# Kernel tuning notes

Hardware: AMD Instinct MI355X
Metric: run time of the kernel (lower is better)

The kernel has to match this reference:

```python
import jax, jax.numpy as jnp
import numpy as np

EPS = 1e-6


def setup_inputs() -> dict:
    key = jax.random.key(0)
    ks = jax.random.split(key, 7)
    T, B, D, N = 512, 32, 1024, 128
    scale_w = (6.0 / (N + D)) ** 0.5  # xavier_uniform bound
    def w(k):
        return jax.random.uniform(k, (N, D), jnp.float32, -scale_w, scale_w)
    return {
        "x": jax.random.normal(ks[0], (T, B, D), jnp.float32),
        "S0": jnp.zeros((B, N, N), jnp.float32),
        "W_k": w(ks[1]),
        "W_v": w(ks[2]),
        "W_q": w(ks[3]),
        "W_erase": w(ks[4]),
        "W_write": w(ks[5]),
    }


def _ntm_forward(x, S0, W_k, W_v, W_q, W_erase, W_write):
    # Projections for all timesteps at once: (T, B, n_state)
    k = jnp.einsum('tbd,nd->tbn', x, W_k)
    v = jnp.einsum('tbd,nd->tbn', x, W_v)
    q = jnp.einsum('tbd,nd->tbn', x, W_q)
    erase = jnp.einsum('tbd,nd->tbn', x, W_erase)  # use_sigmoid=False: raw
    write = jnp.einsum('tbd,nd->tbn', x, W_write)

    def step(S, inp):
        k_t, v_t, q_t, e_t, w_t = inp
        k_norm = k_t / (jnp.linalg.norm(k_t, axis=-1, keepdims=True) + EPS)
        # S: (B, n, n); outer products via broadcasting
        erase_outer = e_t[:, :, None] * k_norm[:, None, :]
        write_outer = (w_t * v_t)[:, :, None] * k_norm[:, None, :]
        S_new = jnp.tanh(S * (1.0 - erase_outer) + write_outer)
        Sq = jnp.einsum('bij,bj->bi', S_new, q_t)
        out = Sq * jax.nn.silu(Sq)
        return S_new, out

    S_final, outputs = jax.lax.scan(step, S0, (k, v, q, erase, write))
    return outputs, S_final


def reference(x, S0, W_k, W_v, W_q, W_erase, W_write):
    return _ntm_forward(x, S0, W_k, W_v, W_q, W_erase, W_write)
```

## Files before the change

kernel.cpp:

```cpp
#include <hip/hip_runtime.h>
#include <hip/hip_bf16.h>


typedef __attribute__((ext_vector_type(8))) short bf16x8;
typedef __attribute__((ext_vector_type(4))) float f32x4;
typedef __attribute__((ext_vector_type(2))) float f32x2;
typedef __attribute__((ext_vector_type(4))) unsigned short u16x4;

static constexpr int T_STEPS = 512;
static constexpr int BATCH   = 32;
static constexpr int DDIM    = 1024;
static constexpr int NDIM    = 128;
static constexpr int LDC     = 5 * NDIM;
static constexpr int MROWS   = T_STEPS * BATCH;
static constexpr int OUT_N   = T_STEPS * BATCH * NDIM;

__device__ __forceinline__ unsigned short rne_bf16(float v) {
    unsigned u = __builtin_bit_cast(unsigned, v);
    u += 0x7FFFu + ((u >> 16) & 1u);
    return (unsigned short)(u >> 16);
}

static constexpr int LSTR = 40;
static constexpr int OA = 0, OB = 128 * LSTR;

__global__ __launch_bounds__(256, 3) void gemm3_kernel(
    const float* __restrict__ x,
    const float* __restrict__ w0, const float* __restrict__ w1,
    const float* __restrict__ w2, const float* __restrict__ w3,
    const float* __restrict__ w4,
    float* __restrict__ C)
{
    __shared__ unsigned short lds[2 * 128 * LSTR];

    const float* Ws[5] = {w0, w1, w2, w3, w4};
    const int id  = blockIdx.x;
    const int xcd = id & 7;
    const int kq  = id >> 3;
    const int bn  = kq % 5;
    const int bm  = (kq / 5) * 8 + xcd;

    const int tid  = threadIdx.x;
    const int wave = tid >> 6, lane = tid & 63;
    const int quad = lane >> 4, l16 = lane & 15;
    const int wm = (wave >> 1) * 64, wn = (wave & 1) * 64;
    const int m0 = bm * 128;
    const float* wsrc = Ws[bn];

    f32x4 acc[4][4];
#pragma unroll
    for (int i = 0; i < 4; ++i)
#pragma unroll
        for (int j = 0; j < 4; ++j) acc[i][j] = (f32x4)(0.0f);

    const int srow = tid >> 3;
    const int sc4  = tid & 7;
    const int fa = (wm + l16) * LSTR + quad * 8;
    const int fb = (wn + l16) * LSTR + quad * 8;

    const float* xp[4];
    const float* wp[4];
#pragma unroll
    for (int i = 0; i < 4; ++i) {
        xp[i] = x    + (size_t)(m0 + srow + i * 32) * DDIM + sc4 * 4;
        wp[i] = wsrc + (size_t)(srow + i * 32) * DDIM + sc4 * 4;
    }

    f32x4 ra[4], rb[4];
#pragma unroll
    for (int i = 0; i < 4; ++i) { ra[i] = *(const f32x4*)xp[i]; rb[i] = *(const f32x4*)wp[i]; }

    for (int kk = 0; kk < 32; ++kk) {
#pragma unroll
        for (int i = 0; i < 4; ++i) {
            u16x4 ha, hb;
#pragma unroll
            for (int j = 0; j < 4; ++j) {
                ha[j] = rne_bf16(ra[i][j]);
                hb[j] = rne_bf16(rb[i][j]);
            }
            const int o = (srow + i * 32) * LSTR + sc4 * 4;
            *(u16x4*)&lds[OA + o] = ha;
            *(u16x4*)&lds[OB + o] = hb;
        }
        __syncthreads();

        const int kn = (kk + 1 < 32) ? kk + 1 : 31;
#pragma unroll
        for (int i = 0; i < 4; ++i) {
            ra[i] = *(const f32x4*)(xp[i] + kn * 32);
            rb[i] = *(const f32x4*)(wp[i] + kn * 32);
        }

        bf16x8 ah[4], bh[4];
#pragma unroll
        for (int i = 0; i < 4; ++i) {
            ah[i] = *(const bf16x8*)&lds[OA + fa + i * 16 * LSTR];
            bh[i] = *(const bf16x8*)&lds[OB + fb + i * 16 * LSTR];
        }
#pragma unroll
        for (int mi = 0; mi < 4; ++mi)
#pragma unroll
            for (int ni = 0; ni < 4; ++ni)
                acc[mi][ni] = __builtin_amdgcn_mfma_f32_16x16x32_bf16(
                    ah[mi], bh[ni], acc[mi][ni], 0, 0, 0);
        __syncthreads();
    }

#pragma unroll
    for (int mi = 0; mi < 4; ++mi)
#pragma unroll
        for (int ni = 0; ni < 4; ++ni) {
            const int row = m0 + wm + mi * 16 + quad * 4;
            const int col = bn * 128 + wn + ni * 16 + l16;
#pragma unroll
            for (int r = 0; r < 4; ++r)
                C[(size_t)(row + r) * LDC + col] = acc[mi][ni][r];
        }
}

__global__ __launch_bounds__(256) void knorm_kernel(float* __restrict__ C)
{
    const int r    = blockIdx.x * 4 + (threadIdx.x >> 6);
    const int lane = threadIdx.x & 63;
    float* base = C + (size_t)r * LDC;

    f32x2 k2 = *(const f32x2*)(base + lane * 2);
    f32x2 v2 = *(const f32x2*)(base + NDIM + lane * 2);
    f32x2 w2 = *(const f32x2*)(base + 4 * NDIM + lane * 2);

    float ss = k2.x * k2.x + k2.y * k2.y;
#pragma unroll
    for (int off = 32; off >= 1; off >>= 1) ss += __shfl_xor(ss, off, 64);
    float inv = __builtin_amdgcn_rcpf(sqrtf(ss) + 1e-6f);

    f32x2 kn = {k2.x * inv, k2.y * inv};
    f32x2 wv = {v2.x * w2.x, v2.y * w2.y};
    *(f32x2*)(base + lane * 2) = kn;
    *(f32x2*)(base + NDIM + lane * 2) = wv;
}

__device__ __forceinline__ float tanh_fast(float xx) {
    float ex = __builtin_amdgcn_exp2f(xx * 2.8853900817779268f);
    float r  = __builtin_amdgcn_rcpf(ex + 1.0f);
    return fmaf(-2.0f, r, 1.0f);
}

template <int CTRL, int RMASK>
__device__ __forceinline__ float dpp_add(float x) {
    int yi = __builtin_amdgcn_update_dpp(
        0, __builtin_bit_cast(int, x), CTRL, RMASK, 0xF, true);
    return x + __builtin_bit_cast(float, yi);
}

__device__ __forceinline__ float dpp_reduce32(float x) {
    x = dpp_add<0xB1,  0xF>(x);
    x = dpp_add<0x4E,  0xF>(x);
    x = dpp_add<0x141, 0xF>(x);
    x = dpp_add<0x140, 0xF>(x);
    x = dpp_add<0x142, 0xA>(x);
    return x;
}

__global__ __launch_bounds__(256) void ntm_scan_kernel(
    const float* __restrict__ C, const float* __restrict__ S0,
    float* __restrict__ out)
{
    const int L    = blockIdx.x;
    const int b    = (L & 7) + 8 * ((L >> 3) & 3);
    const int row  = (L >> 5) * 8 + (threadIdx.x >> 5);
    const int g    = threadIdx.x & 31;
    const int col0 = g * 4;

    f32x4 S = *(const f32x4*)(S0 + ((size_t)b * NDIM + row) * NDIM + col0);

    const size_t STRIDE = (size_t)BATCH * LDC;
    const float* pb = C + (size_t)b * LDC;

    f32x4 kS[8], qS[8];
    float eS[8], wvS[8];

#pragma unroll
    for (int s = 0; s < 4; ++s) {
        const float* p = pb + (size_t)s * STRIDE;
        kS[s]  = *(const f32x4*)(p + col0);
        qS[s]  = *(const f32x4*)(p + 2 * NDIM + col0);
        eS[s]  = p[3 * NDIM + row];
        wvS[s] = p[NDIM + row];
    }

    float* op = out + (size_t)b * NDIM + row;

    for (int ti = 0; ti < T_STEPS / 8; ++ti) {
#pragma unroll
        for (int j = 0; j < 8; ++j) {
            const int t = ti * 8 + j;
            {
                int tp = t + 4;
                if (tp > T_STEPS - 1) tp = T_STEPS - 1;
                const float* p = pb + (size_t)tp * STRIDE;
                const int ps = (j + 4) & 7;
                kS[ps]  = *(const f32x4*)(p + col0);
                qS[ps]  = *(const f32x4*)(p + 2 * NDIM + col0);
                eS[ps]  = p[3 * NDIM + row];
                wvS[ps] = p[NDIM + row];
            }
            float dot = 0.0f;
#pragma unroll
            for (int u = 0; u < 4; ++u) {
                float t0  = fmaf(-eS[j], S[u], wvS[j]);
                float pre = fmaf(kS[j][u], t0, S[u]);
                S[u] = tanh_fast(pre);
                dot = fmaf(S[u], qS[j][u], dot);
            }
            dot = dpp_reduce32(dot);

            if ((threadIdx.x & 31) == 31)
                op[(size_t)t * BATCH * NDIM] = dot;
        }
    }

    *(f32x4*)(out + (size_t)T_STEPS * BATCH * NDIM
              + ((size_t)b * NDIM + row) * NDIM + col0) = S;
}

__global__ __launch_bounds__(256) void silu_kernel(float* __restrict__ out)
{
    const int i = blockIdx.x * 256 + threadIdx.x;
    f32x4 d = ((const f32x4*)out)[i];
    f32x4 y;
#pragma unroll
    for (int j = 0; j < 4; ++j) {
        float sg = __builtin_amdgcn_rcpf(
            1.0f + __builtin_amdgcn_exp2f(-d[j] * 1.4426950408889634f));
        y[j] = d[j] * d[j] * sg;
    }
    ((f32x4*)out)[i] = y;
}

extern "C" void kernel_launch(void* const* d_in, const int* in_sizes, int n_in,
                              void* d_out, int out_size, void* d_ws, size_t ws_size,
                              hipStream_t stream) {
    const float* x  = (const float*)d_in[0];
    const float* S0 = (const float*)d_in[1];
    const float* wk = (const float*)d_in[2];
    const float* wv = (const float*)d_in[3];
    const float* wq = (const float*)d_in[4];
    const float* we = (const float*)d_in[5];
    const float* ww = (const float*)d_in[6];
    float* out = (float*)d_out;
    float* C   = (float*)d_ws;

    gemm3_kernel<<<640, 256, 0, stream>>>(x, wk, wv, wq, we, ww, C);
    knorm_kernel<<<MROWS / 4, 256, 0, stream>>>(C);
    ntm_scan_kernel<<<512, 256, 0, stream>>>(C, S0, out);
    silu_kernel<<<OUT_N / 1024, 256, 0, stream>>>(out);
}
```

Before: 276.3 us.

## Pre-convert weights to bf16 fragment layout, restructure GEMM, fuse SiLU into scan

Adds a kernel that converts the five weight matrices to bf16 once, stored in an MFMA-fragment-ordered layout. The GEMM is replaced by one where each 512-thread block holds a 64-row slab of x in swizzled LDS and computes all five projections, reading B fragments straight from global memory with double buffering. The SiLU gating is fused into the scan's output write, which removes a separate pass over the output, and the scan's prefetch depth drops from 4 to 2 steps. Risks include low occupancy from 128KB of LDS per block, only 256 blocks, and uncached B fragment loads from global memory.

```diff
diff --git a/kernel.cpp b/kernel.cpp
--- a/kernel.cpp
+++ b/kernel.cpp
@@ -6,6 +6,7 @@
 typedef __attribute__((ext_vector_type(4))) float f32x4;
 typedef __attribute__((ext_vector_type(2))) float f32x2;
 typedef __attribute__((ext_vector_type(4))) unsigned short u16x4;
+typedef __attribute__((ext_vector_type(8))) unsigned short u16x8;
 
 static constexpr int T_STEPS = 512;
 static constexpr int BATCH   = 32;
@@ -15,107 +16,133 @@
 static constexpr int MROWS   = T_STEPS * BATCH;
 static constexpr int OUT_N   = T_STEPS * BATCH * NDIM;
 
+static constexpr size_t C_BYTES = (size_t)MROWS * LDC * 4;
+
 __device__ __forceinline__ unsigned short rne_bf16(float v) {
     unsigned u = __builtin_bit_cast(unsigned, v);
     u += 0x7FFFu + ((u >> 16) & 1u);
     return (unsigned short)(u >> 16);
 }
 
-static constexpr int LSTR = 40;
-static constexpr int OA = 0, OB = 128 * LSTR;
-
-__global__ __launch_bounds__(256, 3) void gemm3_kernel(
-    const float* __restrict__ x,
+__global__ __launch_bounds__(256) void wconv_kernel(
     const float* __restrict__ w0, const float* __restrict__ w1,
     const float* __restrict__ w2, const float* __restrict__ w3,
     const float* __restrict__ w4,
+    unsigned short* __restrict__ W2)
+{
+    const int idx = blockIdx.x * 256 + threadIdx.x;
+    const size_t e = (size_t)idx * 4;
+    const int bn = (int)(e >> 17);
+    const int r  = (int)(e & 131071);
+    const int n  = r >> 10;
+    const int k  = r & 1023;
+
+    const float* wp = w0;
+    if (bn == 1) wp = w1;
+    else if (bn == 2) wp = w2;
+    else if (bn == 3) wp = w3;
+    else if (bn == 4) wp = w4;
+
+    f32x4 v = *(const f32x4*)(wp + r);
+    u16x4 h;
+#pragma unroll
+    for (int j = 0; j < 4; ++j) h[j] = rne_bf16(v[j]);
+
+    const int kk   = k >> 5;
+    const int quad = (k >> 3) & 3;
+    const size_t off = ((((size_t)(bn * 32 + kk) * 128 + n) * 4 + quad) * 8) + (k & 7);
+    *(u16x4*)(W2 + off) = h;
+}
+
+__global__ __launch_bounds__(512, 2) void gemm4_kernel(
+    const float* __restrict__ x,
+    const unsigned short* __restrict__ W2,
     float* __restrict__ C)
 {
-    __shared__ unsigned short lds[2 * 128 * LSTR];
-
-    const float* Ws[5] = {w0, w1, w2, w3, w4};
-    const int id  = blockIdx.x;
-    const int xcd = id & 7;
-    const int kq  = id >> 3;
-    const int bn  = kq % 5;
-    const int bm  = (kq / 5) * 8 + xcd;
-
+    __shared__ unsigned short lds[64 * 1024];
+
+    const int m0   = blockIdx.x * 64;
     const int tid  = threadIdx.x;
     const int wave = tid >> 6, lane = tid & 63;
     const int quad = lane >> 4, l16 = lane & 15;
-    const int wm = (wave >> 1) * 64, wn = (wave & 1) * 64;
-    const int m0 = bm * 128;
-    const float* wsrc = Ws[bn];
-
-    f32x4 acc[4][4];
-#pragma unroll
-    for (int i = 0; i < 4; ++i)
-#pragma unroll
-        for (int j = 0; j < 4; ++j) acc[i][j] = (f32x4)(0.0f);
-
-    const int srow = tid >> 3;
-    const int sc4  = tid & 7;
-    const int fa = (wm + l16) * LSTR + quad * 8;
-    const int fb = (wn + l16) * LSTR + quad * 8;
-
-    const float* xp[4];
-    const float* wp[4];
-#pragma unroll
-    for (int i = 0; i < 4; ++i) {
-        xp[i] = x    + (size_t)(m0 + srow + i * 32) * DDIM + sc4 * 4;
-        wp[i] = wsrc + (size_t)(srow + i * 32) * DDIM + sc4 * 4;
-    }
-
-    f32x4 ra[4], rb[4];
-#pragma unroll
-    for (int i = 0; i < 4; ++i) { ra[i] = *(const f32x4*)xp[i]; rb[i] = *(const f32x4*)wp[i]; }
-
-    for (int kk = 0; kk < 32; ++kk) {
-#pragma unroll
-        for (int i = 0; i < 4; ++i) {
-            u16x4 ha, hb;
-#pragma unroll
-            for (int j = 0; j < 4; ++j) {
-                ha[j] = rne_bf16(ra[i][j]);
-                hb[j] = rne_bf16(rb[i][j]);
-            }
-            const int o = (srow + i * 32) * LSTR + sc4 * 4;
-            *(u16x4*)&lds[OA + o] = ha;
-            *(u16x4*)&lds[OB + o] = hb;
-        }
-        __syncthreads();
-
-        const int kn = (kk + 1 < 32) ? kk + 1 : 31;
-#pragma unroll
-        for (int i = 0; i < 4; ++i) {
-            ra[i] = *(const f32x4*)(xp[i] + kn * 32);
-            rb[i] = *(const f32x4*)(wp[i] + kn * 32);
-        }
-
-        bf16x8 ah[4], bh[4];
-#pragma unroll
-        for (int i = 0; i < 4; ++i) {
-            ah[i] = *(const bf16x8*)&lds[OA + fa + i * 16 * LSTR];
-            bh[i] = *(const bf16x8*)&lds[OB + fb + i * 16 * LSTR];
-        }
-#pragma unroll
-        for (int mi = 0; mi < 4; ++mi)
-#pragma unroll
-            for (int ni = 0; ni < 4; ++ni)
-                acc[mi][ni] = __builtin_amdgcn_mfma_f32_16x16x32_bf16(
-                    ah[mi], bh[ni], acc[mi][ni], 0, 0, 0);
-        __syncthreads();
-    }
-
-#pragma unroll
-    for (int mi = 0; mi < 4; ++mi)
-#pragma unroll
-        for (int ni = 0; ni < 4; ++ni) {
-            const int row = m0 + wm + mi * 16 + quad * 4;
-            const int col = bn * 128 + wn + ni * 16 + l16;
+
+    {
+        const int k8 = tid & 127;
+        const int rb = tid >> 7;
+#pragma unroll 4
+        for (int it = 0; it < 16; ++it) {
+            const int row = it * 4 + rb;
+            const float* src = x + (size_t)(m0 + row) * DDIM + k8 * 8;
+            f32x4 v0 = *(const f32x4*)src;
+            f32x4 v1 = *(const f32x4*)(src + 4);
+            u16x8 h;
+            h[0] = rne_bf16(v0[0]); h[1] = rne_bf16(v0[1]);
+            h[2] = rne_bf16(v0[2]); h[3] = rne_bf16(v0[3]);
+            h[4] = rne_bf16(v1[0]); h[5] = rne_bf16(v1[1]);
+            h[6] = rne_bf16(v1[2]); h[7] = rne_bf16(v1[3]);
+            const int byteo = row * 2048 + ((k8 * 16) ^ ((row & 7) << 4));
+            *(u16x8*)((char*)lds + byteo) = h;
+        }
+    }
+    __syncthreads();
+
+    f32x4 acc[5][4];
+#pragma unroll
+    for (int bn = 0; bn < 5; ++bn)
+#pragma unroll
+        for (int mi = 0; mi < 4; ++mi) acc[bn][mi] = (f32x4)(0.0f);
+
+    const int aswz = (l16 & 7) << 4;
+    const unsigned short* bp = W2 + ((size_t)((wave * 16 + l16) * 4 + quad)) * 8;
+
+    auto LDA = [&](int mi, int kk) -> bf16x8 {
+        const int byteo = (mi * 16 + l16) * 2048 + ((kk * 64 + quad * 16) ^ aswz);
+        return *(const bf16x8*)((const char*)lds + byteo);
+    };
+
+    bf16x8 aC[4], bC[5], aN[4], bN[5];
+#pragma unroll
+    for (int mi = 0; mi < 4; ++mi) aC[mi] = LDA(mi, 0);
+#pragma unroll
+    for (int bn = 0; bn < 5; ++bn)
+        bC[bn] = *(const bf16x8*)(bp + (size_t)bn * 131072);
+
+    for (int kk = 0; kk < 32; kk += 2) {
+#pragma unroll
+        for (int mi = 0; mi < 4; ++mi) aN[mi] = LDA(mi, kk + 1);
+#pragma unroll
+        for (int bn = 0; bn < 5; ++bn)
+            bN[bn] = *(const bf16x8*)(bp + (size_t)bn * 131072 + (size_t)(kk + 1) * 4096);
+#pragma unroll
+        for (int bn = 0; bn < 5; ++bn)
+#pragma unroll
+            for (int mi = 0; mi < 4; ++mi)
+                acc[bn][mi] = __builtin_amdgcn_mfma_f32_16x16x32_bf16(
+                    aC[mi], bC[bn], acc[bn][mi], 0, 0, 0);
+        if (kk < 30) {
+#pragma unroll
+            for (int mi = 0; mi < 4; ++mi) aC[mi] = LDA(mi, kk + 2);
+#pragma unroll
+            for (int bn = 0; bn < 5; ++bn)
+                bC[bn] = *(const bf16x8*)(bp + (size_t)bn * 131072 + (size_t)(kk + 2) * 4096);
+        }
+#pragma unroll
+        for (int bn = 0; bn < 5; ++bn)
+#pragma unroll
+            for (int mi = 0; mi < 4; ++mi)
+                acc[bn][mi] = __builtin_amdgcn_mfma_f32_16x16x32_bf16(
+                    aN[mi], bN[bn], acc[bn][mi], 0, 0, 0);
+    }
+
+#pragma unroll
+    for (int bn = 0; bn < 5; ++bn)
+#pragma unroll
+        for (int mi = 0; mi < 4; ++mi) {
+            const int rw = m0 + mi * 16 + quad * 4;
+            const int cl = bn * 128 + wave * 16 + l16;
 #pragma unroll
             for (int r = 0; r < 4; ++r)
-                C[(size_t)(row + r) * LDC + col] = acc[mi][ni][r];
+                C[(size_t)(rw + r) * LDC + cl] = acc[bn][mi][r];
         }
 }
 
@@ -177,11 +204,11 @@
     const size_t STRIDE = (size_t)BATCH * LDC;
     const float* pb = C + (size_t)b * LDC;
 
-    f32x4 kS[8], qS[8];
-    float eS[8], wvS[8];
-
-#pragma unroll
-    for (int s = 0; s < 4; ++s) {
+    f32x4 kS[4], qS[4];
+    float eS[4], wvS[4];
+
+#pragma unroll
+    for (int s = 0; s < 2; ++s) {
         const float* p = pb + (size_t)s * STRIDE;
         kS[s]  = *(const f32x4*)(p + col0);
         qS[s]  = *(const f32x4*)(p + 2 * NDIM + col0);
@@ -191,15 +218,15 @@
 
     float* op = out + (size_t)b * NDIM + row;
 
-    for (int ti = 0; ti < T_STEPS / 8; ++ti) {
-#pragma unroll
-        for (int j = 0; j < 8; ++j) {
-            const int t = ti * 8 + j;
+    for (int ti = 0; ti < T_STEPS / 4; ++ti) {
+#pragma unroll
+        for (int j = 0; j < 4; ++j) {
+            const int t = ti * 4 + j;
             {
-                int tp = t + 4;
+                int tp = t + 2;
                 if (tp > T_STEPS - 1) tp = T_STEPS - 1;
                 const float* p = pb + (size_t)tp * STRIDE;
-                const int ps = (j + 4) & 7;
+                const int ps = (j + 2) & 3;
                 kS[ps]  = *(const f32x4*)(p + col0);
                 qS[ps]  = *(const f32x4*)(p + 2 * NDIM + col0);
                 eS[ps]  = p[3 * NDIM + row];
@@ -215,27 +242,17 @@
             }
             dot = dpp_reduce32(dot);
 
-            if ((threadIdx.x & 31) == 31)
-                op[(size_t)t * BATCH * NDIM] = dot;
+            if ((threadIdx.x & 31) == 31) {
+                const float d = dot;
+                const float sg = __builtin_amdgcn_rcpf(
+                    1.0f + __builtin_amdgcn_exp2f(-d * 1.4426950408889634f));
+                op[(size_t)t * BATCH * NDIM] = d * d * sg;
+            }
         }
     }
 
     *(f32x4*)(out + (size_t)T_STEPS * BATCH * NDIM
               + ((size_t)b * NDIM + row) * NDIM + col0) = S;
-}
-
-__global__ __launch_bounds__(256) void silu_kernel(float* __restrict__ out)
-{
-    const int i = blockIdx.x * 256 + threadIdx.x;
-    f32x4 d = ((const f32x4*)out)[i];
-    f32x4 y;
-#pragma unroll
-    for (int j = 0; j < 4; ++j) {
-        float sg = __builtin_amdgcn_rcpf(
-            1.0f + __builtin_amdgcn_exp2f(-d[j] * 1.4426950408889634f));
-        y[j] = d[j] * d[j] * sg;
-    }
-    ((f32x4*)out)[i] = y;
 }
 
 extern "C" void kernel_launch(void* const* d_in, const int* in_sizes, int n_in,
@@ -250,9 +267,10 @@
     const float* ww = (const float*)d_in[6];
     float* out = (float*)d_out;
     float* C   = (float*)d_ws;
-
-    gemm3_kernel<<<640, 256, 0, stream>>>(x, wk, wv, wq, we, ww, C);
+    unsigned short* W2 = (unsigned short*)((char*)d_ws + C_BYTES);
+
+    wconv_kernel<<<640, 256, 0, stream>>>(wk, wv, wq, we, ww, W2);
+    gemm4_kernel<<<256, 512, 0, stream>>>(x, W2, C);
     knorm_kernel<<<MROWS / 4, 256, 0, stream>>>(C);
     ntm_scan_kernel<<<512, 256, 0, stream>>>(C, S0, out);
-    silu_kernel<<<OUT_N / 1024, 256, 0, stream>>>(out);
-}
+}
```

Measured after the change: 266.5 us. 1.04x faster.
